# Kernel optimization log

Measured on AMD Instinct MI355X. Metric: run time of the kernel, lower is better.

Reference implementation:

```python
import jax, jax.numpy as jnp
import numpy as np

N = 262144
DIM = 256
NUM_HEADS = 4
HEAD_DIM = DIM // NUM_HEADS
B = 4096
SCALE = HEAD_DIM ** (-0.5)
EPS = 1e-8


def setup_inputs() -> dict:
    key = jax.random.key(0)
    ks = jax.random.split(key, 7)
    x = jax.random.normal(ks[0], (N, DIM), dtype=jnp.float32)
    batch = jnp.sort(jax.random.randint(ks[1], (N,), 0, B)).astype(jnp.int64)
    query = jax.random.normal(ks[2], (NUM_HEADS, HEAD_DIM), dtype=jnp.float32)
    # nn.Linear default init scale ~ 1/sqrt(dim); keep exp() well-behaved
    key_w = jax.random.normal(ks[3], (DIM, DIM), dtype=jnp.float32) / np.sqrt(DIM)
    key_b = jax.random.normal(ks[4], (DIM,), dtype=jnp.float32) * 0.01
    value_w = jax.random.normal(ks[5], (DIM, DIM), dtype=jnp.float32) / np.sqrt(DIM)
    value_b = jax.random.normal(ks[6], (DIM,), dtype=jnp.float32) * 0.01
    return {"x": x, "batch": batch, "query": query, "key_w": key_w,
            "key_b": key_b, "value_w": value_w, "value_b": value_b}


def reference(x, batch, query, key_w, key_b, value_w, value_b):
    # k, v: [N, H, Hd]  (torch Linear: x @ W.T + b)
    k = (x @ key_w.T + key_b).reshape(N, NUM_HEADS, HEAD_DIM)
    v = (x @ value_w.T + value_b).reshape(N, NUM_HEADS, HEAD_DIM)
    # attn: [N, H] -- dot of learned per-head query with each node's key
    attn = jnp.einsum('hd,nhd->nh', query, k) * SCALE
    attn_exp = jnp.exp(attn)  # faithful: no max-subtraction in original
    # segment softmax denominator gathered back to nodes: [N, H]
    attn_sum = jax.ops.segment_sum(attn_exp, batch, num_segments=B)[batch]
    attn_norm = attn_exp / (attn_sum + EPS)
    # weighted values scatter-added per segment: [B, H, Hd]
    weighted = attn_norm[:, :, None] * v
    pooled = jax.ops.segment_sum(weighted, batch, num_segments=B)
    return pooled.reshape(B, DIM)
```

## Files before the change

kernel.cpp:

```cpp
#include <hip/hip_runtime.h>


constexpr int DIM = 256;
constexpr int NH  = 4;
constexpr int HD  = 64;
constexpr float SCL  = 0.125f;
constexpr float EPSV = 1e-8f;

constexpr int WS_QW   = 0;
constexpr int WS_QB   = 1024;
constexpr int WS_OFFS = 1088;
constexpr int WS_VWT  = 8192;
constexpr int WS_SRAW = 73728;

__global__ void prep_qw(const float* __restrict__ query,
                        const float* __restrict__ key_w,
                        const float* __restrict__ key_b,
                        float* __restrict__ ws){
  int t = blockIdx.x * 256 + threadIdx.x;
  int h = t >> 8, j = t & 255;
  float acc = 0.f;
  #pragma unroll 8
  for (int d = 0; d < HD; ++d)
    acc += query[h*HD+d] * key_w[(size_t)(h*HD+d)*DIM + j];
  ws[WS_QW + t] = acc;
  if (j == 0){
    float bb = 0.f;
    for (int d = 0; d < HD; ++d)
      bb += query[h*HD+d] * key_b[h*HD+d];
    ws[WS_QB + h] = bb;
  }
}

__global__ void prep_vwt(const float* __restrict__ value_w, float* __restrict__ ws){
  int jj = blockIdx.x;
  int t  = threadIdx.x;
  float4 v = *(const float4*)(value_w + (size_t)t*DIM + 4*jj);
  ((float4*)(ws + WS_VWT))[jj*256 + t] = v;
}

__global__ void seg_offsets(const int* __restrict__ batch32,
                            int* __restrict__ offs, int N, int B){
  int i = blockIdx.x * 256 + threadIdx.x;
  if (i >= N) return;
  const bool is64 = (batch32[N-1] == 0);
  int v  = is64 ? batch32[2*i] : batch32[i];
  int vp = (i == 0) ? -1 : (is64 ? batch32[2*(i-1)] : batch32[i-1]);
  for (int b = vp + 1; b <= v; ++b) offs[b] = i;
  if (i == N-1)
    for (int b = v + 1; b <= B; ++b) offs[b] = N;
}

template<int MODE>
__global__ __launch_bounds__(512, 4)
void attn_pool(const float* __restrict__ x,
               const int* __restrict__ offs,
               const float* __restrict__ ws,
               const float* __restrict__ value_w,
               const float* __restrict__ value_b,
               float* __restrict__ sraw,
               float* __restrict__ esum,
               float* __restrict__ out){
  constexpr int LDSF = (MODE == 0) ? (8192 + 32)
                     : (MODE == 1) ? (8192 + 32 + 1024 + 2048 + 8)
                                   : (8192 + 32 + 1024 + 512 + 8);
  __shared__ __align__(16) float lds[LDSF];
  float* S_all    = lds;
  float* sums_all = lds + 8192;

  const int b   = blockIdx.x;
  const int tid = threadIdx.x;
  const int seg_start = offs[b];
  const int seg_end   = offs[b+1];

  const int wave = tid >> 6, lane = tid & 63;
  const int half = lane >> 5, sl = lane & 31;
  const int sigma = wave * 2 + half;

  float qwr[NH][8];
  #pragma unroll
  for (int h = 0; h < NH; ++h){
    const float4* q4 = (const float4*)(ws + WS_QW + h*DIM + sl*8);
    float4 a = q4[0], c = q4[1];
    qwr[h][0]=a.x; qwr[h][1]=a.y; qwr[h][2]=a.z; qwr[h][3]=a.w;
    qwr[h][4]=c.x; qwr[h][5]=c.y; qwr[h][6]=c.z; qwr[h][7]=c.w;
  }
  float qb[NH];
  #pragma unroll
  for (int h = 0; h < NH; ++h) qb[h] = ws[WS_QB + h];

  float Sacc[NH][8];
  #pragma unroll
  for (int h = 0; h < NH; ++h)
    #pragma unroll
    for (int c = 0; c < 8; ++c) Sacc[h][c] = 0.f;
  float se[NH] = {0.f, 0.f, 0.f, 0.f};

  const float4* xr4 = (const float4*)x;
  const float4 Z = make_float4(0.f, 0.f, 0.f, 0.f);

  int n0 = seg_start + sigma*2;
  bool v0 = n0 < seg_end;
  bool v1 = n0 + 1 < seg_end;
  float4 a0=Z, b0=Z, a1=Z, b1=Z;
  if (v0){ a0 = xr4[(size_t)n0*64 + sl*2];     b0 = xr4[(size_t)n0*64 + sl*2 + 1]; }
  if (v1){ a1 = xr4[(size_t)(n0+1)*64 + sl*2]; b1 = xr4[(size_t)(n0+1)*64 + sl*2 + 1]; }

  while (v0){
    const int nn = n0 + 32;
    const bool w0 = nn < seg_end;
    const bool w1 = nn + 1 < seg_end;
    float4 c0=Z, d0=Z, c1=Z, d1=Z;
    if (w0){ c0 = xr4[(size_t)nn*64 + sl*2];     d0 = xr4[(size_t)nn*64 + sl*2 + 1]; }
    if (w1){ c1 = xr4[(size_t)(nn+1)*64 + sl*2]; d1 = xr4[(size_t)(nn+1)*64 + sl*2 + 1]; }

    float xv0[8] = {a0.x,a0.y,a0.z,a0.w,b0.x,b0.y,b0.z,b0.w};
    float xv1[8] = {a1.x,a1.y,a1.z,a1.w,b1.x,b1.y,b1.z,b1.w};

    float p0[NH], p1[NH];
    #pragma unroll
    for (int h = 0; h < NH; ++h){
      float s0 = 0.f, s1 = 0.f;
      #pragma unroll
      for (int c = 0; c < 8; ++c){ s0 += qwr[h][c]*xv0[c]; s1 += qwr[h][c]*xv1[c]; }
      p0[h] = s0; p1[h] = s1;
    }
    #pragma unroll
    for (int m = 1; m < 32; m <<= 1){
      #pragma unroll
      for (int h = 0; h < NH; ++h){
        p0[h] += __shfl_xor(p0[h], m, 64);
        p1[h] += __shfl_xor(p1[h], m, 64);
      }
    }
    const float g1 = v1 ? 1.f : 0.f;
    #pragma unroll
    for (int h = 0; h < NH; ++h){
      float e0 = __expf((p0[h] + qb[h]) * SCL);
      float e1 = __expf((p1[h] + qb[h]) * SCL) * g1;
      se[h] += e0 + e1;
      #pragma unroll
      for (int c = 0; c < 8; ++c)
        Sacc[h][c] += e0*xv0[c] + e1*xv1[c];
    }
    n0 = nn; v0 = w0; v1 = w1;
    a0 = c0; b0 = d0; a1 = c1; b1 = d1;
  }

  #pragma unroll
  for (int h = 0; h < NH; ++h){
    se[h] += __shfl_xor(se[h], 32, 64);
    #pragma unroll
    for (int c = 0; c < 8; ++c) Sacc[h][c] += __shfl_xor(Sacc[h][c], 32, 64);
  }
  if (half == 0){
    #pragma unroll
    for (int h = 0; h < NH; ++h){
      float4 lo = make_float4(Sacc[h][0], Sacc[h][1], Sacc[h][2], Sacc[h][3]);
      float4 hi = make_float4(Sacc[h][4], Sacc[h][5], Sacc[h][6], Sacc[h][7]);
      float4* dst = (float4*)&S_all[wave*1024 + h*256 + sl*8];
      dst[0] = lo; dst[1] = hi;
    }
    if (sl == 0){
      #pragma unroll
      for (int h = 0; h < NH; ++h) sums_all[wave*4 + h] = se[h];
    }
  }
  __syncthreads();

  if constexpr (MODE == 0){
    #pragma unroll
    for (int k = 0; k < 2; ++k){
      const int idx = tid + k*512;
      float s = 0.f;
      #pragma unroll
      for (int w = 0; w < 8; ++w) s += S_all[w*1024 + idx];
      sraw[(size_t)b*1024 + idx] = s;
    }
    if (tid < NH){
      float tot = 0.f;
      #pragma unroll
      for (int w = 0; w < 8; ++w) tot += sums_all[w*4 + tid];
      esum[b*4 + tid] = tot;
    }
  } else if constexpr (MODE == 1){
    float* Sfin  = lds + 8224;
    float* ep    = lds + 9248;
    float* invs  = lds + 11296;
    float* wsums = lds + 11300;
    #pragma unroll
    for (int k = 0; k < 2; ++k){
      const int idx = tid + k*512;
      float s = 0.f;
      #pragma unroll
      for (int w = 0; w < 8; ++w) s += S_all[w*1024 + idx];
      Sfin[idx] = s;
    }
    if (tid < NH){
      float tot = 0.f;
      #pragma unroll
      for (int w = 0; w < 8; ++w) tot += sums_all[w*4 + tid];
      float inv = 1.f / (tot + EPSV);
      invs[tid] = inv; wsums[tid] = tot * inv;
    }
    __syncthreads();
    const float4* vwt4 = (const float4*)(ws + WS_VWT);
    const int hh = lane >> 4;
    float4 acc = make_float4(0.f, 0.f, 0.f, 0.f);
    for (int jj = wave*8; jj < wave*8 + 8; ++jj){
      float4 q0 = vwt4[jj*256 + 4*lane + 0];
      float4 q1 = vwt4[jj*256 + 4*lane + 1];
      float4 q2 = vwt4[jj*256 + 4*lane + 2];
      float4 q3 = vwt4[jj*256 + 4*lane + 3];
      float4 sf = *(const float4*)&Sfin[hh*256 + 4*jj];
      acc.x += q0.x*sf.x + q0.y*sf.y + q0.z*sf.z + q0.w*sf.w;
      acc.y += q1.x*sf.x + q1.y*sf.y + q1.z*sf.z + q1.w*sf.w;
      acc.z += q2.x*sf.x + q2.y*sf.y + q2.z*sf.z + q2.w*sf.w;
      acc.w += q3.x*sf.x + q3.y*sf.y + q3.z*sf.z + q3.w*sf.w;
    }
    *(float4*)&ep[wave*256 + 4*lane] = acc;
    __syncthreads();
    if (tid < 256){
      const int t = tid, h2 = t >> 6;
      float s = 0.f;
      #pragma unroll
      for (int w = 0; w < 8; ++w) s += ep[w*256 + t];
      out[(size_t)b*256 + t] = s * invs[h2] + wsums[h2] * value_b[t];
    }
  } else {
    float* Sfin  = lds + 8224;
    float* ep2   = lds + 9248;
    float* invs  = lds + 9760;
    float* wsums = lds + 9764;
    #pragma unroll
    for (int k = 0; k < 2; ++k){
      const int idx = tid + k*512;
      float s = 0.f;
      #pragma unroll
      for (int w = 0; w < 8; ++w) s += S_all[w*1024 + idx];
      Sfin[idx] = s;
    }
    if (tid < NH){
      float tot = 0.f;
      #pragma unroll
      for (int w = 0; w < 8; ++w) tot += sums_all[w*4 + tid];
      float inv = 1.f / (tot + EPSV);
      invs[tid] = inv; wsums[tid] = tot * inv;
    }
    __syncthreads();
    const int t = tid & 255, part = tid >> 8;
    const int h2 = t >> 6;
    const float4* vrow = (const float4*)(value_w + (size_t)t * DIM) + part*32;
    const float4* sp   = (const float4*)&Sfin[h2*256] + part*32;
    float acc = 0.f;
    #pragma unroll
    for (int q = 0; q < 32; ++q){
      float4 r = vrow[q];
      float4 s = sp[q];
      acc += r.x*s.x + r.y*s.y + r.z*s.z + r.w*s.w;
    }
    ep2[part*256 + t] = acc;
    __syncthreads();
    if (part == 0)
      out[(size_t)b * DIM + t] = (ep2[t] + ep2[256 + t]) * invs[h2] + wsums[h2] * value_b[t];
  }
}

__global__ __launch_bounds__(256, 4)
void val_proj(const float* __restrict__ ws,
              const float* __restrict__ sraw,
              const float* __restrict__ esum,
              const float* __restrict__ value_b,
              float* __restrict__ out){
  constexpr int TB = 8;
  __shared__ __align__(16) float Sl[NH*DIM*TB];
  const int b0  = blockIdx.x * TB;
  const int tid = threadIdx.x;

  for (int idx = tid; idx < NH*DIM*TB; idx += 256){
    const int i = idx >> 10, rem = idx & 1023;
    Sl[rem*TB + i] = sraw[(size_t)(b0 + i)*1024 + rem];
  }
  __syncthreads();

  const int t = tid, h = t >> 6;
  const float4* vwt4 = (const float4*)(ws + WS_VWT);
  float acc[TB];
  #pragma unroll
  for (int i = 0; i < TB; ++i) acc[i] = 0.f;

  #pragma unroll 4
  for (int jj = 0; jj < 64; ++jj){
    const float4 w4 = vwt4[jj*256 + t];
    #pragma unroll
    for (int r = 0; r < 4; ++r){
      const float* sp = &Sl[(h*256 + 4*jj + r)*TB];
      const float4 s0 = *(const float4*)sp;
      const float4 s1 = *(const float4*)(sp + 4);
      const float wr = (&w4.x)[r];
      acc[0] += wr*s0.x; acc[1] += wr*s0.y; acc[2] += wr*s0.z; acc[3] += wr*s0.w;
      acc[4] += wr*s1.x; acc[5] += wr*s1.y; acc[6] += wr*s1.z; acc[7] += wr*s1.w;
    }
  }
  const float vb = value_b[t];
  #pragma unroll
  for (int i = 0; i < TB; ++i){
    const float es  = esum[(b0 + i)*4 + h];
    const float inv = 1.f / (es + EPSV);
    out[(size_t)(b0 + i)*256 + t] = acc[i]*inv + es*inv*vb;
  }
}

extern "C" void kernel_launch(void* const* d_in, const int* in_sizes, int n_in,
                              void* d_out, int out_size, void* d_ws, size_t ws_size,
                              hipStream_t stream){
  const float* x       = (const float*)d_in[0];
  const int*   batch   = (const int*)d_in[1];
  const float* query   = (const float*)d_in[2];
  const float* key_w   = (const float*)d_in[3];
  const float* key_b   = (const float*)d_in[4];
  const float* value_w = (const float*)d_in[5];
  const float* value_b = (const float*)d_in[6];
  float* ws  = (float*)d_ws;
  float* out = (float*)d_out;

  const int N = in_sizes[1];
  const int B = out_size / DIM;

  int*   offs = (int*)(ws + WS_OFFS);
  float* sraw = ws + WS_SRAW;
  float* esum = ws + WS_SRAW + (size_t)B*1024;

  const size_t need_split = ((size_t)WS_SRAW + (size_t)B*1024 + (size_t)B*4) * sizeof(float);
  const size_t need_vwt   = ((size_t)WS_VWT + 65536) * sizeof(float);

  prep_qw<<<4, 256, 0, stream>>>(query, key_w, key_b, ws);
  seg_offsets<<<(N + 255) / 256, 256, 0, stream>>>(batch, offs, N, B);

  if (ws_size >= need_split){
    prep_vwt<<<64, 256, 0, stream>>>(value_w, ws);
    attn_pool<0><<<B, 512, 0, stream>>>(x, offs, ws, value_w, value_b, sraw, esum, nullptr);
    val_proj<<<B / 8, 256, 0, stream>>>(ws, sraw, esum, value_b, out);
  } else if (ws_size >= need_vwt){
    prep_vwt<<<64, 256, 0, stream>>>(value_w, ws);
    attn_pool<1><<<B, 512, 0, stream>>>(x, offs, ws, value_w, value_b, nullptr, nullptr, out);
  } else {
    attn_pool<2><<<B, 512, 0, stream>>>(x, offs, ws, value_w, value_b, nullptr, nullptr, out);
  }
}
```

Baseline: 407.2 us.

## Split each segment across two 256-thread blocks and change x load layout

The split path now launches two 256-thread blocks per segment, each covering half the nodes and writing its own partial S and exp-sum. val_proj merges the two partials when it loads them. Per-lane x loads change from two adjacent float4s to float4s at lane and lane+32, so each wave instruction reads contiguous memory. The goal is more blocks and better occupancy for the memory-bound streaming of x, at the cost of doubling the partial-result traffic through the workspace.

```diff
diff --git a/kernel.cpp b/kernel.cpp
--- a/kernel.cpp
+++ b/kernel.cpp
@@ -51,18 +51,190 @@
     for (int b = v + 1; b <= B; ++b) offs[b] = N;
 }
 
+__global__ __launch_bounds__(256, 6)
+void attn_pool_split(const float* __restrict__ x,
+                     const int* __restrict__ offs,
+                     const float* __restrict__ ws,
+                     float* __restrict__ sraw,
+                     float* __restrict__ esum){
+  __shared__ __align__(16) float S_all[4][NH*DIM];
+  __shared__ float sums_all[4][NH];
+
+  const int bid = blockIdx.x;
+  const int b   = bid >> 1, part = bid & 1;
+  const int tid = threadIdx.x;
+  const int s = offs[b], e = offs[b+1];
+  const int len = e - s;
+  const int h1  = (len + 1) >> 1;
+  const int ps  = s + part * h1;
+  const int pe  = part ? e : (s + h1);
+
+  const int wave = tid >> 6, lane = tid & 63;
+  const int half = lane >> 5, sl = lane & 31;
+  const int sigma = wave * 2 + half;
+
+  float qwr[NH][8];
+  #pragma unroll
+  for (int h = 0; h < NH; ++h){
+    float4 a = *(const float4*)(ws + WS_QW + h*DIM + 4*sl);
+    float4 c = *(const float4*)(ws + WS_QW + h*DIM + 128 + 4*sl);
+    qwr[h][0]=a.x; qwr[h][1]=a.y; qwr[h][2]=a.z; qwr[h][3]=a.w;
+    qwr[h][4]=c.x; qwr[h][5]=c.y; qwr[h][6]=c.z; qwr[h][7]=c.w;
+  }
+  float qb[NH];
+  #pragma unroll
+  for (int h = 0; h < NH; ++h) qb[h] = ws[WS_QB + h];
+
+  float Sacc[NH][8];
+  #pragma unroll
+  for (int h = 0; h < NH; ++h)
+    #pragma unroll
+    for (int c = 0; c < 8; ++c) Sacc[h][c] = 0.f;
+  float se[NH] = {0.f, 0.f, 0.f, 0.f};
+
+  const float4* xr4 = (const float4*)x;
+  const float4 Z = make_float4(0.f, 0.f, 0.f, 0.f);
+
+  int n0 = ps + sigma*2;
+  bool v0 = n0 < pe;
+  bool v1 = n0 + 1 < pe;
+  float4 a0=Z, b0=Z, a1=Z, b1=Z;
+  if (v0){ a0 = xr4[(size_t)n0*64 + sl];     b0 = xr4[(size_t)n0*64 + 32 + sl]; }
+  if (v1){ a1 = xr4[(size_t)(n0+1)*64 + sl]; b1 = xr4[(size_t)(n0+1)*64 + 32 + sl]; }
+
+  while (v0){
+    const int nn = n0 + 16;
+    const bool w0 = nn < pe;
+    const bool w1 = nn + 1 < pe;
+    float4 c0=Z, d0=Z, c1=Z, d1=Z;
+    if (w0){ c0 = xr4[(size_t)nn*64 + sl];     d0 = xr4[(size_t)nn*64 + 32 + sl]; }
+    if (w1){ c1 = xr4[(size_t)(nn+1)*64 + sl]; d1 = xr4[(size_t)(nn+1)*64 + 32 + sl]; }
+
+    float xv0[8] = {a0.x,a0.y,a0.z,a0.w,b0.x,b0.y,b0.z,b0.w};
+    float xv1[8] = {a1.x,a1.y,a1.z,a1.w,b1.x,b1.y,b1.z,b1.w};
+
+    float p0[NH], p1[NH];
+    #pragma unroll
+    for (int h = 0; h < NH; ++h){
+      float s0 = 0.f, s1 = 0.f;
+      #pragma unroll
+      for (int c = 0; c < 8; ++c){ s0 += qwr[h][c]*xv0[c]; s1 += qwr[h][c]*xv1[c]; }
+      p0[h] = s0; p1[h] = s1;
+    }
+    #pragma unroll
+    for (int m = 1; m < 32; m <<= 1){
+      #pragma unroll
+      for (int h = 0; h < NH; ++h){
+        p0[h] += __shfl_xor(p0[h], m, 64);
+        p1[h] += __shfl_xor(p1[h], m, 64);
+      }
+    }
+    const float g1 = v1 ? 1.f : 0.f;
+    #pragma unroll
+    for (int h = 0; h < NH; ++h){
+      float e0 = __expf((p0[h] + qb[h]) * SCL);
+      float e1 = __expf((p1[h] + qb[h]) * SCL) * g1;
+      se[h] += e0 + e1;
+      #pragma unroll
+      for (int c = 0; c < 8; ++c)
+        Sacc[h][c] += e0*xv0[c] + e1*xv1[c];
+    }
+    n0 = nn; v0 = w0; v1 = w1;
+    a0 = c0; b0 = d0; a1 = c1; b1 = d1;
+  }
+
+  #pragma unroll
+  for (int h = 0; h < NH; ++h){
+    se[h] += __shfl_xor(se[h], 32, 64);
+    #pragma unroll
+    for (int c = 0; c < 8; ++c) Sacc[h][c] += __shfl_xor(Sacc[h][c], 32, 64);
+  }
+  if (half == 0){
+    #pragma unroll
+    for (int h = 0; h < NH; ++h){
+      float4 lo = make_float4(Sacc[h][0], Sacc[h][1], Sacc[h][2], Sacc[h][3]);
+      float4 hi = make_float4(Sacc[h][4], Sacc[h][5], Sacc[h][6], Sacc[h][7]);
+      *(float4*)&S_all[wave][h*DIM + 4*sl]       = lo;
+      *(float4*)&S_all[wave][h*DIM + 128 + 4*sl] = hi;
+    }
+    if (sl == 0){
+      #pragma unroll
+      for (int h = 0; h < NH; ++h) sums_all[wave][h] = se[h];
+    }
+  }
+  __syncthreads();
+
+  #pragma unroll
+  for (int k = 0; k < 4; ++k){
+    const int idx = tid + k*256;
+    float sv = 0.f;
+    #pragma unroll
+    for (int w = 0; w < 4; ++w) sv += S_all[w][idx];
+    sraw[(size_t)bid*1024 + idx] = sv;
+  }
+  if (tid < NH){
+    float tot = 0.f;
+    #pragma unroll
+    for (int w = 0; w < 4; ++w) tot += sums_all[w][tid];
+    esum[bid*4 + tid] = tot;
+  }
+}
+
+__global__ __launch_bounds__(256, 4)
+void val_proj(const float* __restrict__ ws,
+              const float* __restrict__ sraw,
+              const float* __restrict__ esum,
+              const float* __restrict__ value_b,
+              float* __restrict__ out){
+  constexpr int TB = 8;
+  __shared__ __align__(16) float Sl[NH*DIM*TB];
+  const int b0  = blockIdx.x * TB;
+  const int tid = threadIdx.x;
+
+  for (int idx = tid; idx < NH*DIM*TB; idx += 256){
+    const int i = idx >> 10, rem = idx & 1023;
+    const size_t base = (size_t)(b0 + i) * 2048;
+    Sl[rem*TB + i] = sraw[base + rem] + sraw[base + 1024 + rem];
+  }
+  __syncthreads();
+
+  const int t = tid, h = t >> 6;
+  const float4* vwt4 = (const float4*)(ws + WS_VWT);
+  float acc[TB];
+  #pragma unroll
+  for (int i = 0; i < TB; ++i) acc[i] = 0.f;
+
+  #pragma unroll 4
+  for (int jj = 0; jj < 64; ++jj){
+    const float4 w4 = vwt4[jj*256 + t];
+    #pragma unroll
+    for (int r = 0; r < 4; ++r){
+      const float* sp = &Sl[(h*256 + 4*jj + r)*TB];
+      const float4 s0 = *(const float4*)sp;
+      const float4 s1 = *(const float4*)(sp + 4);
+      const float wr = (&w4.x)[r];
+      acc[0] += wr*s0.x; acc[1] += wr*s0.y; acc[2] += wr*s0.z; acc[3] += wr*s0.w;
+      acc[4] += wr*s1.x; acc[5] += wr*s1.y; acc[6] += wr*s1.z; acc[7] += wr*s1.w;
+    }
+  }
+  const float vb = value_b[t];
+  #pragma unroll
+  for (int i = 0; i < TB; ++i){
+    const float es  = esum[(b0 + i)*8 + h] + esum[(b0 + i)*8 + 4 + h];
+    const float inv = 1.f / (es + EPSV);
+    out[(size_t)(b0 + i)*256 + t] = acc[i]*inv + es*inv*vb;
+  }
+}
+
 template<int MODE>
 __global__ __launch_bounds__(512, 4)
-void attn_pool(const float* __restrict__ x,
-               const int* __restrict__ offs,
-               const float* __restrict__ ws,
-               const float* __restrict__ value_w,
-               const float* __restrict__ value_b,
-               float* __restrict__ sraw,
-               float* __restrict__ esum,
-               float* __restrict__ out){
-  constexpr int LDSF = (MODE == 0) ? (8192 + 32)
-                     : (MODE == 1) ? (8192 + 32 + 1024 + 2048 + 8)
+void attn_pool_fused(const float* __restrict__ x,
+                     const int* __restrict__ offs,
+                     const float* __restrict__ ws,
+                     const float* __restrict__ value_w,
+                     const float* __restrict__ value_b,
+                     float* __restrict__ out){
+  constexpr int LDSF = (MODE == 1) ? (8192 + 32 + 1024 + 2048 + 8)
                                    : (8192 + 32 + 1024 + 512 + 8);
   __shared__ __align__(16) float lds[LDSF];
   float* S_all    = lds;
@@ -80,8 +252,8 @@
   float qwr[NH][8];
   #pragma unroll
   for (int h = 0; h < NH; ++h){
-    const float4* q4 = (const float4*)(ws + WS_QW + h*DIM + sl*8);
-    float4 a = q4[0], c = q4[1];
+    float4 a = *(const float4*)(ws + WS_QW + h*DIM + 4*sl);
+    float4 c = *(const float4*)(ws + WS_QW + h*DIM + 128 + 4*sl);
     qwr[h][0]=a.x; qwr[h][1]=a.y; qwr[h][2]=a.z; qwr[h][3]=a.w;
     qwr[h][4]=c.x; qwr[h][5]=c.y; qwr[h][6]=c.z; qwr[h][7]=c.w;
   }
@@ -103,16 +275,16 @@
   bool v0 = n0 < seg_end;
   bool v1 = n0 + 1 < seg_end;
   float4 a0=Z, b0=Z, a1=Z, b1=Z;
-  if (v0){ a0 = xr4[(size_t)n0*64 + sl*2];     b0 = xr4[(size_t)n0*64 + sl*2 + 1]; }
-  if (v1){ a1 = xr4[(size_t)(n0+1)*64 + sl*2]; b1 = xr4[(size_t)(n0+1)*64 + sl*2 + 1]; }
+  if (v0){ a0 = xr4[(size_t)n0*64 + sl];     b0 = xr4[(size_t)n0*64 + 32 + sl]; }
+  if (v1){ a1 = xr4[(size_t)(n0+1)*64 + sl]; b1 = xr4[(size_t)(n0+1)*64 + 32 + sl]; }
 
   while (v0){
     const int nn = n0 + 32;
     const bool w0 = nn < seg_end;
     const bool w1 = nn + 1 < seg_end;
     float4 c0=Z, d0=Z, c1=Z, d1=Z;
-    if (w0){ c0 = xr4[(size_t)nn*64 + sl*2];     d0 = xr4[(size_t)nn*64 + sl*2 + 1]; }
-    if (w1){ c1 = xr4[(size_t)(nn+1)*64 + sl*2]; d1 = xr4[(size_t)(nn+1)*64 + sl*2 + 1]; }
+    if (w0){ c0 = xr4[(size_t)nn*64 + sl];     d0 = xr4[(size_t)nn*64 + 32 + sl]; }
+    if (w1){ c1 = xr4[(size_t)(nn+1)*64 + sl]; d1 = xr4[(size_t)(nn+1)*64 + 32 + sl]; }
 
     float xv0[8] = {a0.x,a0.y,a0.z,a0.w,b0.x,b0.y,b0.z,b0.w};
     float xv1[8] = {a1.x,a1.y,a1.z,a1.w,b1.x,b1.y,b1.z,b1.w};
@@ -158,8 +330,8 @@
     for (int h = 0; h < NH; ++h){
       float4 lo = make_float4(Sacc[h][0], Sacc[h][1], Sacc[h][2], Sacc[h][3]);
       float4 hi = make_float4(Sacc[h][4], Sacc[h][5], Sacc[h][6], Sacc[h][7]);
-      float4* dst = (float4*)&S_all[wave*1024 + h*256 + sl*8];
-      dst[0] = lo; dst[1] = hi;
+      *(float4*)&S_all[wave*1024 + h*DIM + 4*sl]       = lo;
+      *(float4*)&S_all[wave*1024 + h*DIM + 128 + 4*sl] = hi;
     }
     if (sl == 0){
       #pragma unroll
@@ -168,42 +340,28 @@
   }
   __syncthreads();
 
-  if constexpr (MODE == 0){
-    #pragma unroll
-    for (int k = 0; k < 2; ++k){
-      const int idx = tid + k*512;
-      float s = 0.f;
-      #pragma unroll
-      for (int w = 0; w < 8; ++w) s += S_all[w*1024 + idx];
-      sraw[(size_t)b*1024 + idx] = s;
-    }
-    if (tid < NH){
-      float tot = 0.f;
-      #pragma unroll
-      for (int w = 0; w < 8; ++w) tot += sums_all[w*4 + tid];
-      esum[b*4 + tid] = tot;
-    }
-  } else if constexpr (MODE == 1){
-    float* Sfin  = lds + 8224;
-    float* ep    = lds + 9248;
-    float* invs  = lds + 11296;
-    float* wsums = lds + 11300;
-    #pragma unroll
-    for (int k = 0; k < 2; ++k){
-      const int idx = tid + k*512;
-      float s = 0.f;
-      #pragma unroll
-      for (int w = 0; w < 8; ++w) s += S_all[w*1024 + idx];
-      Sfin[idx] = s;
-    }
-    if (tid < NH){
-      float tot = 0.f;
-      #pragma unroll
-      for (int w = 0; w < 8; ++w) tot += sums_all[w*4 + tid];
-      float inv = 1.f / (tot + EPSV);
-      invs[tid] = inv; wsums[tid] = tot * inv;
-    }
-    __syncthreads();
+  float* Sfin  = lds + 8224;
+  float* invs  = (MODE == 1) ? lds + 11296 : lds + 9760;
+  float* wsums = invs + 4;
+  #pragma unroll
+  for (int k = 0; k < 2; ++k){
+    const int idx = tid + k*512;
+    float sv = 0.f;
+    #pragma unroll
+    for (int w = 0; w < 8; ++w) sv += S_all[w*1024 + idx];
+    Sfin[idx] = sv;
+  }
+  if (tid < NH){
+    float tot = 0.f;
+    #pragma unroll
+    for (int w = 0; w < 8; ++w) tot += sums_all[w*4 + tid];
+    float inv = 1.f / (tot + EPSV);
+    invs[tid] = inv; wsums[tid] = tot * inv;
+  }
+  __syncthreads();
+
+  if constexpr (MODE == 1){
+    float* ep = lds + 9248;
     const float4* vwt4 = (const float4*)(ws + WS_VWT);
     const int hh = lane >> 4;
     float4 acc = make_float4(0.f, 0.f, 0.f, 0.f);
@@ -222,32 +380,13 @@
     __syncthreads();
     if (tid < 256){
       const int t = tid, h2 = t >> 6;
-      float s = 0.f;
-      #pragma unroll
-      for (int w = 0; w < 8; ++w) s += ep[w*256 + t];
-      out[(size_t)b*256 + t] = s * invs[h2] + wsums[h2] * value_b[t];
+      float sv = 0.f;
+      #pragma unroll
+      for (int w = 0; w < 8; ++w) sv += ep[w*256 + t];
+      out[(size_t)b*256 + t] = sv * invs[h2] + wsums[h2] * value_b[t];
     }
   } else {
-    float* Sfin  = lds + 8224;
-    float* ep2   = lds + 9248;
-    float* invs  = lds + 9760;
-    float* wsums = lds + 9764;
-    #pragma unroll
-    for (int k = 0; k < 2; ++k){
-      const int idx = tid + k*512;
-      float s = 0.f;
-      #pragma unroll
-      for (int w = 0; w < 8; ++w) s += S_all[w*1024 + idx];
-      Sfin[idx] = s;
-    }
-    if (tid < NH){
-      float tot = 0.f;
-      #pragma unroll
-      for (int w = 0; w < 8; ++w) tot += sums_all[w*4 + tid];
-      float inv = 1.f / (tot + EPSV);
-      invs[tid] = inv; wsums[tid] = tot * inv;
-    }
-    __syncthreads();
+    float* ep2 = lds + 9248;
     const int t = tid & 255, part = tid >> 8;
     const int h2 = t >> 6;
     const float4* vrow = (const float4*)(value_w + (size_t)t * DIM) + part*32;
@@ -256,58 +395,13 @@
     #pragma unroll
     for (int q = 0; q < 32; ++q){
       float4 r = vrow[q];
-      float4 s = sp[q];
-      acc += r.x*s.x + r.y*s.y + r.z*s.z + r.w*s.w;
+      float4 sv = sp[q];
+      acc += r.x*sv.x + r.y*sv.y + r.z*sv.z + r.w*sv.w;
     }
     ep2[part*256 + t] = acc;
     __syncthreads();
     if (part == 0)
       out[(size_t)b * DIM + t] = (ep2[t] + ep2[256 + t]) * invs[h2] + wsums[h2] * value_b[t];
-  }
-}
-
-__global__ __launch_bounds__(256, 4)
-void val_proj(const float* __restrict__ ws,
-              const float* __restrict__ sraw,
-              const float* __restrict__ esum,
-              const float* __restrict__ value_b,
-              float* __restrict__ out){
-  constexpr int TB = 8;
-  __shared__ __align__(16) float Sl[NH*DIM*TB];
-  const int b0  = blockIdx.x * TB;
-  const int tid = threadIdx.x;
-
-  for (int idx = tid; idx < NH*DIM*TB; idx += 256){
-    const int i = idx >> 10, rem = idx & 1023;
-    Sl[rem*TB + i] = sraw[(size_t)(b0 + i)*1024 + rem];
-  }
-  __syncthreads();
-
-  const int t = tid, h = t >> 6;
-  const float4* vwt4 = (const float4*)(ws + WS_VWT);
-  float acc[TB];
-  #pragma unroll
-  for (int i = 0; i < TB; ++i) acc[i] = 0.f;
-
-  #pragma unroll 4
-  for (int jj = 0; jj < 64; ++jj){
-    const float4 w4 = vwt4[jj*256 + t];
-    #pragma unroll
-    for (int r = 0; r < 4; ++r){
-      const float* sp = &Sl[(h*256 + 4*jj + r)*TB];
-      const float4 s0 = *(const float4*)sp;
-      const float4 s1 = *(const float4*)(sp + 4);
-      const float wr = (&w4.x)[r];
-      acc[0] += wr*s0.x; acc[1] += wr*s0.y; acc[2] += wr*s0.z; acc[3] += wr*s0.w;
-      acc[4] += wr*s1.x; acc[5] += wr*s1.y; acc[6] += wr*s1.z; acc[7] += wr*s1.w;
-    }
-  }
-  const float vb = value_b[t];
-  #pragma unroll
-  for (int i = 0; i < TB; ++i){
-    const float es  = esum[(b0 + i)*4 + h];
-    const float inv = 1.f / (es + EPSV);
-    out[(size_t)(b0 + i)*256 + t] = acc[i]*inv + es*inv*vb;
   }
 }
 
@@ -329,9 +423,9 @@
 
   int*   offs = (int*)(ws + WS_OFFS);
   float* sraw = ws + WS_SRAW;
-  float* esum = ws + WS_SRAW + (size_t)B*1024;
-
-  const size_t need_split = ((size_t)WS_SRAW + (size_t)B*1024 + (size_t)B*4) * sizeof(float);
+  float* esum = ws + WS_SRAW + (size_t)B*2048;
+
+  const size_t need_split = ((size_t)WS_SRAW + (size_t)B*2048 + (size_t)B*8) * sizeof(float);
   const size_t need_vwt   = ((size_t)WS_VWT + 65536) * sizeof(float);
 
   prep_qw<<<4, 256, 0, stream>>>(query, key_w, key_b, ws);
@@ -339,12 +433,12 @@
 
   if (ws_size >= need_split){
     prep_vwt<<<64, 256, 0, stream>>>(value_w, ws);
-    attn_pool<0><<<B, 512, 0, stream>>>(x, offs, ws, value_w, value_b, sraw, esum, nullptr);
+    attn_pool_split<<<2*B, 256, 0, stream>>>(x, offs, ws, sraw, esum);
     val_proj<<<B / 8, 256, 0, stream>>>(ws, sraw, esum, value_b, out);
   } else if (ws_size >= need_vwt){
     prep_vwt<<<64, 256, 0, stream>>>(value_w, ws);
-    attn_pool<1><<<B, 512, 0, stream>>>(x, offs, ws, value_w, value_b, nullptr, nullptr, out);
+    attn_pool_fused<1><<<B, 512, 0, stream>>>(x, offs, ws, value_w, value_b, out);
   } else {
-    attn_pool<2><<<B, 512, 0, stream>>>(x, offs, ws, value_w, value_b, nullptr, nullptr, out);
-  }
-}
+    attn_pool_fused<2><<<B, 512, 0, stream>>>(x, offs, ws, value_w, value_b, out);
+  }
+}
```

Result: slower. 706.2 us (+73.4%).
